# Kernel optimization log

Hardware: AMD Instinct MI355X
Metric: run time of the kernel (lower is better)

The kernel has to match this reference:

```python
import jax, jax.numpy as jnp
import numpy as np

N, E, L, H, C, F, NCLASS, NGRAPH = 50000, 800000, 3, 2, 64, 128, 10, 64
NEG_SLOPE = 0.2


def setup_inputs() -> dict:
    key = jax.random.key(0)
    ks = jax.random.split(key, 8)
    x = jax.random.normal(ks[0], (N, F), dtype=jnp.float32)
    edge_index = jax.random.randint(ks[1], (2, E), 0, N, dtype=jnp.int64)
    batch = jnp.sort(jax.random.randint(ks[2], (N,), 0, NGRAPH, dtype=jnp.int64))
    s = 1.0 / np.sqrt(F)
    W = jax.random.normal(ks[3], (L, F, H * C), dtype=jnp.float32) * s
    att_src = jax.random.normal(ks[4], (L, H, C), dtype=jnp.float32) * s
    att_dst = jax.random.normal(ks[5], (L, H, C), dtype=jnp.float32) * s
    bias = jnp.zeros((L, H * C), dtype=jnp.float32)
    lin_w = jax.random.normal(ks[6], (H * C, NCLASS), dtype=jnp.float32) * s
    lin_b = jnp.zeros((NCLASS,), dtype=jnp.float32)
    return {"x": x, "edge_index": edge_index, "batch": batch, "W": W,
            "att_src": att_src, "att_dst": att_dst, "bias": bias,
            "lin_w": lin_w, "lin_b": lin_b}


def _gat_layer(x, src, dst, w, a_s, a_d, b):
    n = x.shape[0]
    h = (x @ w).reshape(n, H, C)                      # [N,H,C]
    alpha_src = jnp.sum(h * a_s, axis=-1)             # [N,H]
    alpha_dst = jnp.sum(h * a_d, axis=-1)             # [N,H]
    e = jax.nn.leaky_relu(alpha_src[src] + alpha_dst[dst], NEG_SLOPE)  # [E2,H]
    # scatter-softmax over incoming edges of each destination node
    m = jax.ops.segment_max(e, dst, num_segments=n)
    p = jnp.exp(e - m[dst])
    z = jax.ops.segment_sum(p, dst, num_segments=n)
    alpha = p / z[dst]                                # [E2,H]
    msg = h[src] * alpha[:, :, None]                  # [E2,H,C]
    out = jax.ops.segment_sum(msg, dst, num_segments=n)  # [N,H,C]
    return out.reshape(n, H * C) + b


def reference(x, edge_index, batch, W, att_src, att_dst, bias, lin_w, lin_b):
    n = x.shape[0]
    # PyG GATConv default: add self-loops
    loop = jnp.arange(n, dtype=edge_index.dtype)
    src = jnp.concatenate([edge_index[0], loop])
    dst = jnp.concatenate([edge_index[1], loop])
    for l in range(L):
        x = _gat_layer(x, src, dst, W[l], att_src[l], att_dst[l], bias[l])
        x = jax.nn.elu(x)  # activation; dropout/bn inactive (eval, use_bn=False)
    # global mean pool per graph
    sums = jax.ops.segment_sum(x, batch, num_segments=NGRAPH)
    cnt = jax.ops.segment_sum(jnp.ones((n,), x.dtype), batch, num_segments=NGRAPH)
    pooled = sums / jnp.maximum(cnt, 1.0)[:, None]    # [NGRAPH, H*C]
    logits = pooled @ lin_w + lin_b
    return jax.nn.softmax(logits, axis=1)
```

## Files before the change

kernel.cpp:

```cpp
#include <hip/hip_runtime.h>
#include <math.h>

#define NNODES 50000
#define NEDGES 800000
#define NLAYERS 3
#define NHEADS 2
#define NCH 64
#define FDIM 128
#define NCLS 10
#define NGRAPH 64
#define NEG_SLOPE 0.2f
#define GEMMB ((NNODES + 63) / 64)
#define NB 391
#define RADB 391
#define PCH 8

#define WAVE_SYNC()                      \
  do {                                   \
    __builtin_amdgcn_wave_barrier();     \
    __asm__ volatile("" ::: "memory");   \
  } while (0)

typedef __attribute__((ext_vector_type(8))) short bf16x8;
typedef __attribute__((ext_vector_type(4))) float f32x4;

__device__ __forceinline__ unsigned short f2bf(float f) {
  unsigned int u = __builtin_bit_cast(unsigned int, f);
  unsigned int r = u + 0x7FFFu + ((u >> 16) & 1u);
  return (unsigned short)(r >> 16);
}
__device__ __forceinline__ float bflo(unsigned v) {
  return __builtin_bit_cast(float, v << 16);
}
__device__ __forceinline__ float bfhi(unsigned v) {
  return __builtin_bit_cast(float, v & 0xFFFF0000u);
}

__global__ __launch_bounds__(256) void k_wprep(const float* __restrict__ W,
                                               unsigned* __restrict__ Wt,
                                               const int* __restrict__ batch,
                                               int* __restrict__ goff,
                                               float* __restrict__ gsum,
                                               int* __restrict__ bcnt) {
  __shared__ float Lt[128][132];
  int l = blockIdx.x;
  int t = threadIdx.x;
  if (l == NLAYERS) {
    if (t < NGRAPH) {
      int lo = 0, hi = NNODES;
      while (lo < hi) {
        int mid = (lo + hi) >> 1;
        if (batch[mid] < t) lo = mid + 1;
        else hi = mid;
      }
      goff[t] = lo;
    }
    if (t == 0) goff[NGRAPH] = NNODES;
    for (int i = t; i < NGRAPH * FDIM; i += 256) gsum[i] = 0.f;
    for (int i = t; i < NB; i += 256) bcnt[i] = 0;
    return;
  }
  const float* Wl = W + (size_t)l * FDIM * FDIM;
  unsigned* Wtl = Wt + (size_t)l * FDIM * FDIM / 2;
#pragma unroll
  for (int i = 0; i < 16; ++i) {
    int k = (t >> 5) + 8 * i;
    int n4 = (t & 31) * 4;
    float4 v = *(const float4*)(Wl + (size_t)k * 128 + n4);
    Lt[k][n4 + 0] = v.x;
    Lt[k][n4 + 1] = v.y;
    Lt[k][n4 + 2] = v.z;
    Lt[k][n4 + 3] = v.w;
  }
  __syncthreads();
  int n = t >> 1;
  int kh = (t & 1) * 64;
  for (int kk = 0; kk < 64; kk += 2) {
    unsigned pk = (unsigned)f2bf(Lt[kh + kk][n]) |
                  ((unsigned)f2bf(Lt[kh + kk + 1][n]) << 16);
    Wtl[n * 64 + (kh >> 1) + (kk >> 1)] = pk;
  }
}

__device__ __forceinline__ void gemm_body(int blk, const float* __restrict__ X,
                                          const unsigned* __restrict__ Wt,
                                          const float* __restrict__ a_sL,
                                          const float* __restrict__ a_dL,
                                          unsigned* __restrict__ Hb,
                                          float* __restrict__ as_,
                                          float* __restrict__ ad_) {
  int t = threadIdx.x;
  int lane = t & 63;
  int w = t >> 6;
  int row0 = blk * 64;
  int n16 = lane & 15;
  int quad = lane >> 4;
  int m0 = w * 16;

  int gr = row0 + m0 + n16;
  const float* xp = X + (size_t)min(gr, NNODES - 1) * 128;

  f32x4 acc[8];
#pragma unroll
  for (int nt = 0; nt < 8; ++nt) {
    f32x4 z = {0.f, 0.f, 0.f, 0.f};
    acc[nt] = z;
  }
#pragma unroll
  for (int kk = 0; kk < 4; ++kk) {
    float4 va = *(const float4*)(xp + kk * 32 + quad * 8);
    float4 vb = *(const float4*)(xp + kk * 32 + quad * 8 + 4);
    bf16x8 af;
    af[0] = (short)f2bf(va.x); af[1] = (short)f2bf(va.y);
    af[2] = (short)f2bf(va.z); af[3] = (short)f2bf(va.w);
    af[4] = (short)f2bf(vb.x); af[5] = (short)f2bf(vb.y);
    af[6] = (short)f2bf(vb.z); af[7] = (short)f2bf(vb.w);
#pragma unroll
    for (int nt = 0; nt < 8; ++nt) {
      bf16x8 bf = *(const bf16x8*)(Wt + (size_t)(nt * 16 + n16) * 64 +
                                   kk * 16 + quad * 4);
      acc[nt] =
          __builtin_amdgcn_mfma_f32_16x16x32_bf16(af, bf, acc[nt], 0, 0, 0);
    }
  }

  float asv[8], adv[8];
#pragma unroll
  for (int nt = 0; nt < 8; ++nt) {
    asv[nt] = a_sL[nt * 16 + n16];
    adv[nt] = a_dL[nt * 16 + n16];
  }
#pragma unroll
  for (int r = 0; r < 4; ++r) {
    int row = row0 + m0 + quad * 4 + r;
    bool ok = (row < NNODES);
    float ps0 = 0.f, pd0 = 0.f, ps1 = 0.f, pd1 = 0.f;
#pragma unroll
    for (int nt = 0; nt < 4; ++nt) {
      ps0 += acc[nt][r] * asv[nt];
      pd0 += acc[nt][r] * adv[nt];
      ps1 += acc[nt + 4][r] * asv[nt + 4];
      pd1 += acc[nt + 4][r] * adv[nt + 4];
    }
#pragma unroll
    for (int off = 1; off < 16; off <<= 1) {
      ps0 += __shfl_xor(ps0, off, 64);
      pd0 += __shfl_xor(pd0, off, 64);
      ps1 += __shfl_xor(ps1, off, 64);
      pd1 += __shfl_xor(pd1, off, 64);
    }
    if (ok && n16 == 0) {
      as_[row * 2 + 0] = ps0;
      as_[row * 2 + 1] = ps1;
      ad_[row * 2 + 0] = pd0;
      ad_[row * 2 + 1] = pd1;
    }
    if (ok) {
#pragma unroll
      for (int nt = 0; nt < 4; ++nt) {
        unsigned pk = (unsigned)f2bf(acc[nt][r]) |
                      ((unsigned)f2bf(acc[nt + 4][r]) << 16);
        Hb[(size_t)row * 64 + nt * 16 + n16] = pk;
      }
    }
  }
}

__global__ __launch_bounds__(256) void k_gemm(const float* __restrict__ X,
                                              const unsigned* __restrict__ Wt,
                                              const float* __restrict__ a_sL,
                                              const float* __restrict__ a_dL,
                                              unsigned* __restrict__ Hb,
                                              float* __restrict__ as_,
                                              float* __restrict__ ad_) {
  gemm_body(blockIdx.x, X, Wt, a_sL, a_dL, Hb, as_, ad_);
}

__global__ __launch_bounds__(256) void k_front(
    const float* __restrict__ X, const unsigned* __restrict__ Wt,
    const float* __restrict__ a_sL, const float* __restrict__ a_dL,
    unsigned* __restrict__ Hb, float* __restrict__ as_,
    float* __restrict__ ad_, const int* __restrict__ ei, int* __restrict__ bh,
    int* __restrict__ bcnt) {
  int b = blockIdx.x;
  if (b < GEMMB) {
    gemm_body(b, X, Wt, a_sL, a_dL, Hb, as_, ad_);
  } else {
    __shared__ int hist[NB];
    int blk = b - GEMMB;
    int t = threadIdx.x;
    for (int i = t; i < NB; i += 256) hist[i] = 0;
    __syncthreads();
    int e0 = blk * 2048;
#pragma unroll
    for (int i = 0; i < 8; ++i) {
      int e = e0 + i * 256 + t;
      if (e < NEDGES) atomicAdd(&hist[ei[NEDGES + e] >> 7], 1);
    }
    __syncthreads();
    for (int i = t; i < NB; i += 256) {
      int c = hist[i];
      int base = c ? atomicAdd(&bcnt[i], c) : 0;
      bh[i * RADB + blk] = base;
    }
  }
}

__global__ __launch_bounds__(256) void k_bscan(const int* __restrict__ bcnt,
                                               int* __restrict__ bstart) {
  __shared__ int ps[256];
  int t = threadIdx.x;
  int x0 = (2 * t < NB) ? bcnt[2 * t] : 0;
  int x1 = (2 * t + 1 < NB) ? bcnt[2 * t + 1] : 0;
  int pair = x0 + x1;
  ps[t] = pair;
  __syncthreads();
  for (int off = 1; off < 256; off <<= 1) {
    int v = (t >= off) ? ps[t - off] : 0;
    __syncthreads();
    ps[t] += v;
    __syncthreads();
  }
  int ex = ps[t] - pair;
  if (2 * t < NB) bstart[2 * t] = ex;
  if (2 * t + 1 < NB) bstart[2 * t + 1] = ex + x0;
  if (t == 0) bstart[NB] = NEDGES;
}

__global__ __launch_bounds__(256) void k_passB(const int* __restrict__ ei,
                                               const int* __restrict__ bstart,
                                               const int* __restrict__ bh,
                                               unsigned* __restrict__ ebuf) {
  __shared__ int curs[NB];
  int blk = blockIdx.x, t = threadIdx.x;
  for (int i = t; i < NB; i += 256) curs[i] = bstart[i] + bh[i * RADB + blk];
  __syncthreads();
  int e0 = blk * 2048;
#pragma unroll
  for (int i = 0; i < 8; ++i) {
    int e = e0 + i * 256 + t;
    if (e < NEDGES) {
      int s = ei[e];
      int d = ei[NEDGES + e];
      int pos = atomicAdd(&curs[d >> 7], 1);
      ebuf[pos] = ((unsigned)s << 7) | (unsigned)(d & 127);
    }
  }
}

__global__ __launch_bounds__(256) void k_passC(const unsigned* __restrict__ ebuf,
                                               const int* __restrict__ bstart,
                                               int* __restrict__ row_ptr,
                                               int* __restrict__ csr) {
  __shared__ int deg[128];
  __shared__ int scn[128];
  int b = blockIdx.x, t = threadIdx.x;
  int node0 = b * 128;
  int nn = min(128, NNODES - node0);
  int estart = bstart[b];
  int eend = bstart[b + 1];
  if (t < 128) deg[t] = 0;
  __syncthreads();
  for (int e = estart + t; e < eend; e += 256)
    atomicAdd(&deg[ebuf[e] & 127], 1);
  __syncthreads();
  if (t < 128) scn[t] = (t < nn) ? deg[t] + 1 : 0;
  __syncthreads();
  for (int off = 1; off < 128; off <<= 1) {
    int v = (t < 128 && t >= off) ? scn[t - off] : 0;
    __syncthreads();
    if (t < 128) scn[t] += v;
    __syncthreads();
  }
  int base = estart + node0;
  if (t < nn) {
    int st = base + (t ? scn[t - 1] : 0);
    row_ptr[node0 + t] = st;
    csr[st] = node0 + t;
    deg[t] = st + 1;
  }
  if (b == 0 && t == 0) row_ptr[NNODES] = NEDGES + NNODES;
  __syncthreads();
  for (int e = estart + t; e < eend; e += 256) {
    unsigned v = ebuf[e];
    int pos = atomicAdd(&deg[v & 127], 1);
    csr[pos] = (int)(v >> 7);
  }
}

__global__ __launch_bounds__(256) void k_aggregate(
    const unsigned* __restrict__ Hb, const float* __restrict__ as_,
    const float* __restrict__ ad_, const int* __restrict__ row_ptr,
    const int* __restrict__ csr, const float* __restrict__ bias,
    float* __restrict__ Xout) {
  __shared__ float2 wb[4][64];
  __shared__ int sb[4][64];
  int wv = threadIdx.x >> 6;
  int lane = threadIdx.x & 63;
  int node = blockIdx.x * 4 + wv;
  if (node >= NNODES) return;
  int rs = row_ptr[node], re = row_ptr[node + 1];
  float2 adv = *(const float2*)&ad_[node * 2];
  const unsigned* Hl = Hb + lane;

  float z0 = 0.f, z1 = 0.f, acc0 = 0.f, acc1 = 0.f;
  for (int base = rs; base < re; base += 64) {
    int j = base + lane;
    float p0 = 0.f, p1 = 0.f;
    int s = 0;
    if (j < re) {
      s = csr[j];
      float2 asv = *(const float2*)&as_[s * 2];
      float e0 = asv.x + adv.x; e0 = (e0 > 0.f) ? e0 : NEG_SLOPE * e0;
      float e1 = asv.y + adv.y; e1 = (e1 > 0.f) ? e1 : NEG_SLOPE * e1;
      p0 = __expf(e0);
      p1 = __expf(e1);
    }
    z0 += p0;
    z1 += p1;
    wb[wv][lane] = make_float2(p0, p1);
    sb[wv][lane] = s;
    WAVE_SYNC();
    int cl = min(64, re - base);
    int cl8 = (cl + 7) & ~7;
    unsigned va[8];
#pragma unroll
    for (int u = 0; u < 8; ++u) va[u] = Hl[(size_t)sb[wv][u] * 64];
    int jj = 8;
    for (; jj < cl8; jj += 8) {
      unsigned vb2[8];
#pragma unroll
      for (int u = 0; u < 8; ++u) vb2[u] = Hl[(size_t)sb[wv][jj + u] * 64];
#pragma unroll
      for (int u = 0; u < 8; ++u) {
        float2 w = wb[wv][jj - 8 + u];
        acc0 += w.x * bflo(va[u]);
        acc1 += w.y * bfhi(va[u]);
      }
#pragma unroll
      for (int u = 0; u < 8; ++u) va[u] = vb2[u];
    }
#pragma unroll
    for (int u = 0; u < 8; ++u) {
      float2 w = wb[wv][jj - 8 + u];
      acc0 += w.x * bflo(va[u]);
      acc1 += w.y * bfhi(va[u]);
    }
    WAVE_SYNC();
  }
#pragma unroll
  for (int off = 32; off > 0; off >>= 1) {
    z0 += __shfl_xor(z0, off, 64);
    z1 += __shfl_xor(z1, off, 64);
  }
  float o0 = acc0 / z0 + bias[lane];
  float o1 = acc1 / z1 + bias[64 + lane];
  o0 = (o0 > 0.f) ? o0 : expm1f(o0);
  o1 = (o1 > 0.f) ? o1 : expm1f(o1);
  Xout[(size_t)node * 128 + lane] = o0;
  Xout[(size_t)node * 128 + 64 + lane] = o1;
}

__global__ __launch_bounds__(256) void k_pool2(const float* __restrict__ Xf,
                                               const int* __restrict__ goff,
                                               float* __restrict__ gsum) {
  __shared__ float red[128];
  int b = blockIdx.x;
  int g = b >> 3, ch = b & 7;
  int t = threadIdx.x;
  int c = t & 127, rh = t >> 7;
  int s = goff[g], e = goff[g + 1];
  int len = e - s;
  int c0 = s + (len * ch) / PCH;
  int c1 = s + (len * (ch + 1)) / PCH;
  float acc = 0.f;
  for (int n = c0 + rh; n < c1; n += 2) acc += Xf[(size_t)n * 128 + c];
  if (rh) red[c] = acc;
  __syncthreads();
  if (!rh) atomicAdd(&gsum[g * FDIM + c], acc + red[c]);
}

__global__ __launch_bounds__(64) void k_final(const float* __restrict__ gsum,
                                              const int* __restrict__ goff,
                                              const float* __restrict__ lw,
                                              const float* __restrict__ lb,
                                              float* __restrict__ out) {
  int g = threadIdx.x;
  float cnt = (float)(goff[g + 1] - goff[g]);
  float inv = 1.f / fmaxf(cnt, 1.f);
  float lg[NCLS];
#pragma unroll
  for (int k = 0; k < NCLS; ++k) lg[k] = lb[k];
  for (int c = 0; c < FDIM; ++c) {
    float pv = gsum[g * FDIM + c] * inv;
#pragma unroll
    for (int k = 0; k < NCLS; ++k) lg[k] += pv * lw[c * NCLS + k];
  }
  float mx = lg[0];
#pragma unroll
  for (int k = 1; k < NCLS; ++k) mx = fmaxf(mx, lg[k]);
  float s = 0.f;
#pragma unroll
  for (int k = 0; k < NCLS; ++k) {
    lg[k] = expf(lg[k] - mx);
    s += lg[k];
  }
  float invs = 1.f / s;
#pragma unroll
  for (int k = 0; k < NCLS; ++k) out[g * NCLS + k] = lg[k] * invs;
}


extern "C" void kernel_launch(void* const* d_in, const int* in_sizes, int n_in,
                              void* d_out, int out_size, void* d_ws,
                              size_t ws_size, hipStream_t stream) {
  const float* x = (const float*)d_in[0];
  const int* ei = (const int*)d_in[1];
  const int* batch = (const int*)d_in[2];
  const float* W = (const float*)d_in[3];
  const float* a_s = (const float*)d_in[4];
  const float* a_d = (const float*)d_in[5];
  const float* bias = (const float*)d_in[6];
  const float* lw = (const float*)d_in[7];
  const float* lb = (const float*)d_in[8];
  float* out = (float*)d_out;

  unsigned* Hb = (unsigned*)d_ws;
  float* xb = (float*)(Hb + (size_t)NNODES * 64);
  float* as_ = xb + (size_t)NNODES * 128;
  float* ad_ = as_ + (size_t)NNODES * 2;
  float* gsum = ad_ + (size_t)NNODES * 2;
  int* goff = (int*)(gsum + NGRAPH * FDIM);
  int* bcnt = goff + (NGRAPH + 1);
  int* bstart = bcnt + NB;
  int* row_ptr = bstart + (NB + 1);
  int* csr = row_ptr + (NNODES + 1);
  int* bh = csr + (NEDGES + NNODES);
  unsigned* ebuf = (unsigned*)(bh + NB * RADB);
  unsigned* Wt = ebuf + (NEDGES + 1024);

  k_wprep<<<NLAYERS + 1, 256, 0, stream>>>(W, Wt, batch, goff, gsum, bcnt);
  k_front<<<GEMMB + RADB, 256, 0, stream>>>(x, Wt, a_s, a_d, Hb, as_, ad_, ei,
                                            bh, bcnt);
  k_bscan<<<1, 256, 0, stream>>>(bcnt, bstart);
  k_passB<<<RADB, 256, 0, stream>>>(ei, bstart, bh, ebuf);
  k_passC<<<NB, 256, 0, stream>>>(ebuf, bstart, row_ptr, csr);

  for (int l = 0; l < NLAYERS; ++l) {
    if (l > 0) {
      k_gemm<<<GEMMB, 256, 0, stream>>>(xb, Wt + (size_t)l * FDIM * FDIM / 2,
                                        a_s + l * FDIM, a_d + l * FDIM, Hb,
                                        as_, ad_);
    }
    k_aggregate<<<(NNODES + 3) / 4, 256, 0, stream>>>(
        Hb, as_, ad_, row_ptr, csr, bias + l * FDIM, xb);
  }
  k_pool2<<<NGRAPH * PCH, 256, 0, stream>>>(xb, goff, gsum);
  k_final<<<1, 64, 0, stream>>>(gsum, goff, lw, lb, out);
}
```

Baseline: 315.8 us.

## Fold attention projections into GEMM, merge scan into passB, fuse pooling

```diff
diff --git a/kernel.cpp b/kernel.cpp
--- a/kernel.cpp
+++ b/kernel.cpp
@@ -13,7 +13,7 @@
 #define GEMMB ((NNODES + 63) / 64)
 #define NB 391
 #define RADB 391
-#define PCH 8
+#define WTL (144 * 64)
 
 #define WAVE_SYNC()                      \
   do {                                   \
@@ -29,6 +29,12 @@
   unsigned int r = u + 0x7FFFu + ((u >> 16) & 1u);
   return (unsigned short)(r >> 16);
 }
+__device__ __forceinline__ float bf16f(unsigned short h) {
+  return __builtin_bit_cast(float, ((unsigned)h) << 16);
+}
+__device__ __forceinline__ float rbf(float x) {
+  return bf16f(f2bf(x));
+}
 __device__ __forceinline__ float bflo(unsigned v) {
   return __builtin_bit_cast(float, v << 16);
 }
@@ -41,8 +47,11 @@
                                                const int* __restrict__ batch,
                                                int* __restrict__ goff,
                                                float* __restrict__ gsum,
-                                               int* __restrict__ bcnt) {
+                                               int* __restrict__ bcnt,
+                                               const float* __restrict__ a_s,
+                                               const float* __restrict__ a_d) {
   __shared__ float Lt[128][132];
+  __shared__ float ex[4][128];
   int l = blockIdx.x;
   int t = threadIdx.x;
   if (l == NLAYERS) {
@@ -61,7 +70,7 @@
     return;
   }
   const float* Wl = W + (size_t)l * FDIM * FDIM;
-  unsigned* Wtl = Wt + (size_t)l * FDIM * FDIM / 2;
+  unsigned* Wtl = Wt + (size_t)l * WTL;
 #pragma unroll
   for (int i = 0; i < 16; ++i) {
     int k = (t >> 5) + 8 * i;
@@ -73,6 +82,23 @@
     Lt[k][n4 + 3] = v.w;
   }
   __syncthreads();
+  if (t < 128) {
+    const float* As = a_s + (size_t)l * FDIM;
+    const float* Ad = a_d + (size_t)l * FDIM;
+    float s0 = 0.f, s1 = 0.f, d0 = 0.f, d1 = 0.f;
+    for (int c = 0; c < 64; ++c) {
+      float w0 = rbf(Lt[t][c]);
+      s0 += w0 * As[c];
+      d0 += w0 * Ad[c];
+      float w1 = rbf(Lt[t][64 + c]);
+      s1 += w1 * As[64 + c];
+      d1 += w1 * Ad[64 + c];
+    }
+    ex[0][t] = s0;
+    ex[1][t] = s1;
+    ex[2][t] = d0;
+    ex[3][t] = d1;
+  }
   int n = t >> 1;
   int kh = (t & 1) * 64;
   for (int kk = 0; kk < 64; kk += 2) {
@@ -80,12 +106,32 @@
                   ((unsigned)f2bf(Lt[kh + kk + 1][n]) << 16);
     Wtl[n * 64 + (kh >> 1) + (kk >> 1)] = pk;
   }
+  __syncthreads();
+  if (t < 32) {
+    int nn = 128 + (t >> 1);
+    int kh2 = (t & 1) * 64;
+    int j = (nn - 128) >> 1;
+    bool lo_ = (nn & 1);
+    for (int kk = 0; kk < 64; kk += 2) {
+      unsigned short w0 = 0, w1 = 0;
+      if (j < 4) {
+        float v0 = ex[j][kh2 + kk], v1 = ex[j][kh2 + kk + 1];
+        unsigned short h0 = f2bf(v0), h1 = f2bf(v1);
+        if (lo_) {
+          w0 = f2bf(v0 - bf16f(h0));
+          w1 = f2bf(v1 - bf16f(h1));
+        } else {
+          w0 = h0;
+          w1 = h1;
+        }
+      }
+      Wtl[nn * 64 + (kh2 >> 1) + (kk >> 1)] = (unsigned)w0 | ((unsigned)w1 << 16);
+    }
+  }
 }
 
 __device__ __forceinline__ void gemm_body(int blk, const float* __restrict__ X,
                                           const unsigned* __restrict__ Wt,
-                                          const float* __restrict__ a_sL,
-                                          const float* __restrict__ a_dL,
                                           unsigned* __restrict__ Hb,
                                           float* __restrict__ as_,
                                           float* __restrict__ ad_) {
@@ -100,9 +146,9 @@
   int gr = row0 + m0 + n16;
   const float* xp = X + (size_t)min(gr, NNODES - 1) * 128;
 
-  f32x4 acc[8];
-#pragma unroll
-  for (int nt = 0; nt < 8; ++nt) {
+  f32x4 acc[9];
+#pragma unroll
+  for (int nt = 0; nt < 9; ++nt) {
     f32x4 z = {0.f, 0.f, 0.f, 0.f};
     acc[nt] = z;
   }
@@ -116,7 +162,7 @@
     af[4] = (short)f2bf(vb.x); af[5] = (short)f2bf(vb.y);
     af[6] = (short)f2bf(vb.z); af[7] = (short)f2bf(vb.w);
 #pragma unroll
-    for (int nt = 0; nt < 8; ++nt) {
+    for (int nt = 0; nt < 9; ++nt) {
       bf16x8 bf = *(const bf16x8*)(Wt + (size_t)(nt * 16 + n16) * 64 +
                                    kk * 16 + quad * 4);
       acc[nt] =
@@ -124,38 +170,16 @@
     }
   }
 
-  float asv[8], adv[8];
-#pragma unroll
-  for (int nt = 0; nt < 8; ++nt) {
-    asv[nt] = a_sL[nt * 16 + n16];
-    adv[nt] = a_dL[nt * 16 + n16];
-  }
 #pragma unroll
   for (int r = 0; r < 4; ++r) {
     int row = row0 + m0 + quad * 4 + r;
     bool ok = (row < NNODES);
-    float ps0 = 0.f, pd0 = 0.f, ps1 = 0.f, pd1 = 0.f;
-#pragma unroll
-    for (int nt = 0; nt < 4; ++nt) {
-      ps0 += acc[nt][r] * asv[nt];
-      pd0 += acc[nt][r] * adv[nt];
-      ps1 += acc[nt + 4][r] * asv[nt + 4];
-      pd1 += acc[nt + 4][r] * adv[nt + 4];
-    }
-#pragma unroll
-    for (int off = 1; off < 16; off <<= 1) {
-      ps0 += __shfl_xor(ps0, off, 64);
-      pd0 += __shfl_xor(pd0, off, 64);
-      ps1 += __shfl_xor(ps1, off, 64);
-      pd1 += __shfl_xor(pd1, off, 64);
-    }
-    if (ok && n16 == 0) {
-      as_[row * 2 + 0] = ps0;
-      as_[row * 2 + 1] = ps1;
-      ad_[row * 2 + 0] = pd0;
-      ad_[row * 2 + 1] = pd1;
-    }
+    float v = acc[8][r] + __shfl_xor(acc[8][r], 1, 64);
     if (ok) {
+      if ((n16 & 1) == 0 && n16 < 8) {
+        float* dp = (n16 & 4) ? ad_ : as_;
+        dp[row * 2 + ((n16 >> 1) & 1)] = v;
+      }
 #pragma unroll
       for (int nt = 0; nt < 4; ++nt) {
         unsigned pk = (unsigned)f2bf(acc[nt][r]) |
@@ -168,23 +192,20 @@
 
 __global__ __launch_bounds__(256) void k_gemm(const float* __restrict__ X,
                                               const unsigned* __restrict__ Wt,
-                                              const float* __restrict__ a_sL,
-                                              const float* __restrict__ a_dL,
                                               unsigned* __restrict__ Hb,
                                               float* __restrict__ as_,
                                               float* __restrict__ ad_) {
-  gemm_body(blockIdx.x, X, Wt, a_sL, a_dL, Hb, as_, ad_);
+  gemm_body(blockIdx.x, X, Wt, Hb, as_, ad_);
 }
 
 __global__ __launch_bounds__(256) void k_front(
     const float* __restrict__ X, const unsigned* __restrict__ Wt,
-    const float* __restrict__ a_sL, const float* __restrict__ a_dL,
     unsigned* __restrict__ Hb, float* __restrict__ as_,
     float* __restrict__ ad_, const int* __restrict__ ei, int* __restrict__ bh,
     int* __restrict__ bcnt) {
   int b = blockIdx.x;
   if (b < GEMMB) {
-    gemm_body(b, X, Wt, a_sL, a_dL, Hb, as_, ad_);
+    gemm_body(b, X, Wt, Hb, as_, ad_);
   } else {
     __shared__ int hist[NB];
     int blk = b - GEMMB;
@@ -206,10 +227,14 @@
   }
 }
 
-__global__ __launch_bounds__(256) void k_bscan(const int* __restrict__ bcnt,
+__global__ __launch_bounds__(256) void k_passB(const int* __restrict__ ei,
+                                               const int* __restrict__ bcnt,
+                                               const int* __restrict__ bh,
+                                               unsigned* __restrict__ ebuf,
                                                int* __restrict__ bstart) {
+  __shared__ int curs[NB];
   __shared__ int ps[256];
-  int t = threadIdx.x;
+  int blk = blockIdx.x, t = threadIdx.x;
   int x0 = (2 * t < NB) ? bcnt[2 * t] : 0;
   int x1 = (2 * t + 1 < NB) ? bcnt[2 * t + 1] : 0;
   int pair = x0 + x1;
@@ -222,18 +247,15 @@
     __syncthreads();
   }
   int ex = ps[t] - pair;
-  if (2 * t < NB) bstart[2 * t] = ex;
-  if (2 * t + 1 < NB) bstart[2 * t + 1] = ex + x0;
-  if (t == 0) bstart[NB] = NEDGES;
-}
-
-__global__ __launch_bounds__(256) void k_passB(const int* __restrict__ ei,
-                                               const int* __restrict__ bstart,
-                                               const int* __restrict__ bh,
-                                               unsigned* __restrict__ ebuf) {
-  __shared__ int curs[NB];
-  int blk = blockIdx.x, t = threadIdx.x;
-  for (int i = t; i < NB; i += 256) curs[i] = bstart[i] + bh[i * RADB + blk];
+  if (2 * t < NB) {
+    curs[2 * t] = ex + bh[(2 * t) * RADB + blk];
+    if (blk == 0) bstart[2 * t] = ex;
+  }
+  if (2 * t + 1 < NB) {
+    curs[2 * t + 1] = ex + x0 + bh[(2 * t + 1) * RADB + blk];
+    if (blk == 0) bstart[2 * t + 1] = ex + x0;
+  }
+  if (blk == 0 && t == 0) bstart[NB] = NEDGES;
   __syncthreads();
   int e0 = blk * 2048;
 #pragma unroll
@@ -292,7 +314,8 @@
     const unsigned* __restrict__ Hb, const float* __restrict__ as_,
     const float* __restrict__ ad_, const int* __restrict__ row_ptr,
     const int* __restrict__ csr, const float* __restrict__ bias,
-    float* __restrict__ Xout) {
+    float* __restrict__ Xout, const int* __restrict__ batchp,
+    float* __restrict__ gsum) {
   __shared__ float2 wb[4][64];
   __shared__ int sb[4][64];
   int wv = threadIdx.x >> 6;
@@ -357,27 +380,14 @@
   float o1 = acc1 / z1 + bias[64 + lane];
   o0 = (o0 > 0.f) ? o0 : expm1f(o0);
   o1 = (o1 > 0.f) ? o1 : expm1f(o1);
-  Xout[(size_t)node * 128 + lane] = o0;
-  Xout[(size_t)node * 128 + 64 + lane] = o1;
-}
-
-__global__ __launch_bounds__(256) void k_pool2(const float* __restrict__ Xf,
-                                               const int* __restrict__ goff,
-                                               float* __restrict__ gsum) {
-  __shared__ float red[128];
-  int b = blockIdx.x;
-  int g = b >> 3, ch = b & 7;
-  int t = threadIdx.x;
-  int c = t & 127, rh = t >> 7;
-  int s = goff[g], e = goff[g + 1];
-  int len = e - s;
-  int c0 = s + (len * ch) / PCH;
-  int c1 = s + (len * (ch + 1)) / PCH;
-  float acc = 0.f;
-  for (int n = c0 + rh; n < c1; n += 2) acc += Xf[(size_t)n * 128 + c];
-  if (rh) red[c] = acc;
-  __syncthreads();
-  if (!rh) atomicAdd(&gsum[g * FDIM + c], acc + red[c]);
+  if (batchp) {
+    int g = batchp[node];
+    atomicAdd(&gsum[g * FDIM + lane], o0);
+    atomicAdd(&gsum[g * FDIM + 64 + lane], o1);
+  } else {
+    Xout[(size_t)node * 128 + lane] = o0;
+    Xout[(size_t)node * 128 + 64 + lane] = o1;
+  }
 }
 
 __global__ __launch_bounds__(64) void k_final(const float* __restrict__ gsum,
@@ -439,22 +449,19 @@
   unsigned* ebuf = (unsigned*)(bh + NB * RADB);
   unsigned* Wt = ebuf + (NEDGES + 1024);
 
-  k_wprep<<<NLAYERS + 1, 256, 0, stream>>>(W, Wt, batch, goff, gsum, bcnt);
-  k_front<<<GEMMB + RADB, 256, 0, stream>>>(x, Wt, a_s, a_d, Hb, as_, ad_, ei,
-                                            bh, bcnt);
-  k_bscan<<<1, 256, 0, stream>>>(bcnt, bstart);
-  k_passB<<<RADB, 256, 0, stream>>>(ei, bstart, bh, ebuf);
+  k_wprep<<<NLAYERS + 1, 256, 0, stream>>>(W, Wt, batch, goff, gsum, bcnt, a_s,
+                                           a_d);
+  k_front<<<GEMMB + RADB, 256, 0, stream>>>(x, Wt, Hb, as_, ad_, ei, bh, bcnt);
+  k_passB<<<RADB, 256, 0, stream>>>(ei, bcnt, bh, ebuf, bstart);
   k_passC<<<NB, 256, 0, stream>>>(ebuf, bstart, row_ptr, csr);
 
   for (int l = 0; l < NLAYERS; ++l) {
     if (l > 0) {
-      k_gemm<<<GEMMB, 256, 0, stream>>>(xb, Wt + (size_t)l * FDIM * FDIM / 2,
-                                        a_s + l * FDIM, a_d + l * FDIM, Hb,
-                                        as_, ad_);
-    }
+      k_gemm<<<GEMMB, 256, 0, stream>>>(xb, Wt + (size_t)l * WTL, Hb, as_, ad_);
+    }
+    const int* bp = (l == NLAYERS - 1) ? batch : nullptr;
     k_aggregate<<<(NNODES + 3) / 4, 256, 0, stream>>>(
-        Hb, as_, ad_, row_ptr, csr, bias + l * FDIM, xb);
-  }
-  k_pool2<<<NGRAPH * PCH, 256, 0, stream>>>(xb, goff, gsum);
+        Hb, as_, ad_, row_ptr, csr, bias + l * FDIM, xb, bp, gsum);
+  }
   k_final<<<1, 64, 0, stream>>>(gsum, goff, lw, lb, out);
 }
```

New measurement: 360.8 us. +14.3%, slower.
